# Optimization experiments

Hardware: AMD Instinct MI355X
Metric: run time of the kernel (lower is better)

Reference implementation:

```python
import jax, jax.numpy as jnp
import numpy as np

V = 50257; E = 1024; H = 1024; L = 256; NL = 2; D = 10


def setup_inputs() -> dict:
    key = jax.random.key(0)
    ks = jax.random.split(key, 16)
    n = lambda k, s: jax.random.normal(k, s, dtype=jnp.float32)
    return {
        "input_tok": jax.random.randint(ks[0], (1, 1), 0, V),
        "h0": n(ks[1], (NL, 1, H)),
        "c0": n(ks[2], (NL, 1, H)),
        "h_s": n(ks[3], (L, 1, H)),
        "h_t_tilde": n(ks[4], (1, 1, H)),
        "emb": n(ks[5], (V, E)) * 0.02,
        "Wp": n(ks[6], (H, H)) * (H ** -0.5),
        "wdot": n(ks[7], (1, H)) * (H ** -0.5),
        "Wbil": n(ks[8], (1, H, H)) * (H ** -0.5),
        "Wcomb": n(ks[9], (H, 2 * H)) * ((2 * H) ** -0.5),
        "bcomb": jnp.zeros((H,), jnp.float32),
        "Wih0": n(ks[10], (4 * H, E + H)) * ((E + H) ** -0.5),
        "Whh0": n(ks[11], (4 * H, H)) * (H ** -0.5),
        "bih0": jnp.zeros((4 * H,), jnp.float32),
        "bhh0": jnp.zeros((4 * H,), jnp.float32),
        "Wih1": n(ks[12], (4 * H, H)) * (H ** -0.5),
        "Whh1": n(ks[13], (4 * H, H)) * (H ** -0.5),
        "bih1": jnp.zeros((4 * H,), jnp.float32),
        "bhh1": jnp.zeros((4 * H,), jnp.float32),
        "Wout": n(ks[14], (V, H)) * (H ** -0.5),
        "bout": jnp.zeros((V,), jnp.float32),
    }


def _lstm_cell(x, h, c, Wih, Whh, bih, bhh):
    # torch LSTM gate order: i, f, g, o
    g = x @ Wih.T + bih + h @ Whh.T + bhh
    i, f, gg, o = jnp.split(g, 4, axis=-1)
    c2 = jax.nn.sigmoid(f) * c + jax.nn.sigmoid(i) * jnp.tanh(gg)
    h2 = jax.nn.sigmoid(o) * jnp.tanh(c2)
    return h2, c2


def reference(input_tok, h0, c0, h_s, h_t_tilde, emb, Wp, wdot, Wbil, Wcomb, bcomb,
              Wih0, Whh0, bih0, bhh0, Wih1, Whh1, bih1, bhh1, Wout, bout):
    embedding = emb[input_tok]                                  # [1,1,E]
    x = jnp.concatenate((embedding, h_t_tilde), axis=-1)[0]     # [1,E+H]
    h1, c1 = _lstm_cell(x, h0[0], c0[0], Wih0, Whh0, bih0, bhh0)
    h2, c2 = _lstm_cell(h1, h0[1], c0[1], Wih1, Whh1, bih1, bhh1)
    h_new = jnp.stack((h1, h2)); c_new = jnp.stack((c1, c2))
    h_t = h2                                                    # [1,H]
    Ls = h_s.shape[0]
    p_t = Ls * jax.nn.sigmoid(jnp.tanh(h_t @ Wp.T) @ wdot.T).squeeze()  # scalar
    s = jnp.round(p_t).astype(jnp.int32)
    idx = jnp.arange(Ls)
    lo = jnp.maximum(s - D, 0); hi = jnp.minimum(s + D, Ls - 1)
    mask = (idx >= lo) & (idx <= hi)                            # [L] local window
    # bilinear score h_t^T W h_s over all positions; mask outside window
    score = jnp.einsum('bh,ohk,lbk->lbo', h_t, Wbil, h_s)       # [L,1,1]
    neg = jnp.finfo(score.dtype).min
    a = jax.nn.softmax(jnp.where(mask[:, None, None], score, neg), axis=0)
    # NOTE: original uses exp(+d^2/(D/2)^2) (no minus sign); replicated faithfully.
    expo = jnp.where(mask, ((idx.astype(jnp.float32) - p_t) ** 2) / ((D / 2) ** 2), 0.0)
    a_t = a * jnp.exp(expo)[:, None, None]                      # [L,1,1]
    win = (hi - lo + 1).astype(jnp.float32)
    context = jnp.sum(a_t * h_s, axis=0, keepdims=True) / win   # [1,1,H] (mean over window)
    cat = jnp.concatenate((context, h_t[None]), axis=-1)        # [1,1,2H]
    h_t_tilde_new = jnp.tanh(cat @ Wcomb.T + bcomb)             # [1,1,H]
    y = jax.nn.log_softmax(h_t_tilde_new @ Wout.T + bout, axis=-1)  # [1,1,V]
    return (y, h_new, c_new, h_t_tilde_new, a_t, p_t)
```

## Files before the change

### kernel.cpp

```cpp
#include <hip/hip_runtime.h>
#include <math.h>

#define V 50257
#define E 1024
#define HH 1024
#define LL 256

#define O_H  (V)
#define O_C  (V + 2*HH)
#define O_HT (V + 4*HH)
#define O_A  (V + 5*HH)
#define O_P  (V + 5*HH + LL)

#define W_T    0
#define W_V    1024
#define W_H1   2048
#define W_H2   3072
#define W_Z    4096
#define W_BM   54400
#define W_BS   55424

#define NWL   8192
#define MAXR  7

__device__ __forceinline__ float sigmoidf_(float x) { return 1.f / (1.f + expf(-x)); }
__device__ __forceinline__ float dot4(float4 a, float4 b) {
    return a.x * b.x + a.y * b.y + a.z * b.z + a.w * b.w;
}

__device__ __forceinline__ float block_sum(float v, float* red) {
    int lane = threadIdx.x & 63, wv = threadIdx.x >> 6;
#pragma unroll
    for (int o = 32; o > 0; o >>= 1) v += __shfl_down(v, o, 64);
    __syncthreads();
    if (lane == 0) red[wv] = v;
    __syncthreads();
    return red[0] + red[1] + red[2] + red[3];
}

__global__ __launch_bounds__(512) void k_lstmA(
    const float* __restrict__ Wih0, const float* __restrict__ Whh0,
    const float* __restrict__ Whh1,
    const float* __restrict__ bih0, const float* __restrict__ bhh0,
    const float* __restrict__ emb, const int* __restrict__ tok,
    const float* __restrict__ htt,
    const float* __restrict__ h0, const float* __restrict__ c0,
    float* __restrict__ h1o, float* __restrict__ c1o, float* __restrict__ h1w,
    float* __restrict__ p1, float* __restrict__ vzero) {
    const int u = blockIdx.x, tid = threadIdx.x;
    if (tid == 0) vzero[u] = 0.f;
    const float4* xa4 = (const float4*)(emb + (size_t)tok[0] * E);
    const float4* xb4 = (const float4*)htt;
    const float4* r0 = (const float4*)(Wih0 + (size_t)u * 2048);
    const float4* r1 = (const float4*)(Wih0 + (size_t)(u + HH) * 2048);
    const float4* r2 = (const float4*)(Wih0 + (size_t)(u + 2*HH) * 2048);
    const float4* r3 = (const float4*)(Wih0 + (size_t)(u + 3*HH) * 2048);
    float4 xv = (tid < 256) ? xa4[tid] : xb4[tid - 256];
    float a0 = dot4(r0[tid], xv), a1 = dot4(r1[tid], xv);
    float a2 = dot4(r2[tid], xv), a3 = dot4(r3[tid], xv);
    float b0 = 0.f, b1 = 0.f, b2 = 0.f, b3 = 0.f;
    if (tid < 256) {
        const float4* s0 = (const float4*)(Whh0 + (size_t)u * HH);
        const float4* s1 = (const float4*)(Whh0 + (size_t)(u + HH) * HH);
        const float4* s2 = (const float4*)(Whh0 + (size_t)(u + 2*HH) * HH);
        const float4* s3 = (const float4*)(Whh0 + (size_t)(u + 3*HH) * HH);
        float4 hv = ((const float4*)h0)[tid];
        a0 += dot4(s0[tid], hv); a1 += dot4(s1[tid], hv);
        a2 += dot4(s2[tid], hv); a3 += dot4(s3[tid], hv);
    } else {
        int j = tid - 256;
        const float4* t0 = (const float4*)(Whh1 + (size_t)u * HH);
        const float4* t1 = (const float4*)(Whh1 + (size_t)(u + HH) * HH);
        const float4* t2 = (const float4*)(Whh1 + (size_t)(u + 2*HH) * HH);
        const float4* t3 = (const float4*)(Whh1 + (size_t)(u + 3*HH) * HH);
        float4 gv = ((const float4*)(h0 + HH))[j];
        b0 = dot4(t0[j], gv); b1 = dot4(t1[j], gv);
        b2 = dot4(t2[j], gv); b3 = dot4(t3[j], gv);
    }
    const int lane = tid & 63, wv = tid >> 6;
#pragma unroll
    for (int o = 32; o > 0; o >>= 1) {
        a0 += __shfl_down(a0, o, 64); a1 += __shfl_down(a1, o, 64);
        a2 += __shfl_down(a2, o, 64); a3 += __shfl_down(a3, o, 64);
        b0 += __shfl_down(b0, o, 64); b1 += __shfl_down(b1, o, 64);
        b2 += __shfl_down(b2, o, 64); b3 += __shfl_down(b3, o, 64);
    }
    __shared__ float sma[8][4], smb[8][4];
    if (lane == 0) {
        sma[wv][0] = a0; sma[wv][1] = a1; sma[wv][2] = a2; sma[wv][3] = a3;
        smb[wv][0] = b0; smb[wv][1] = b1; smb[wv][2] = b2; smb[wv][3] = b3;
    }
    __syncthreads();
    if (tid == 0) {
        float g[4], p[4];
#pragma unroll
        for (int i = 0; i < 4; ++i) {
            float ga = 0.f, pb = 0.f;
#pragma unroll
            for (int w = 0; w < 8; ++w) { ga += sma[w][i]; pb += smb[w][i]; }
            g[i] = ga + bih0[u + i*HH] + bhh0[u + i*HH];
            p[i] = pb;
        }
        float c = sigmoidf_(g[1]) * c0[u] + sigmoidf_(g[0]) * tanhf(g[2]);
        float h = sigmoidf_(g[3]) * tanhf(c);
        h1o[u] = h; c1o[u] = c; h1w[u] = h;
        p1[u*4+0] = p[0]; p1[u*4+1] = p[1]; p1[u*4+2] = p[2]; p1[u*4+3] = p[3];
    }
}

__global__ void k_lstmB(
    const float* __restrict__ Wih1,
    const float* __restrict__ bih1, const float* __restrict__ bhh1,
    const float* __restrict__ h1w, const float* __restrict__ p1,
    const float* __restrict__ h0, const float* __restrict__ c0,
    float* __restrict__ h2o, float* __restrict__ c2o, float* __restrict__ h2w) {
    const int u = blockIdx.x, tid = threadIdx.x;
    const float4* r0 = (const float4*)(Wih1 + (size_t)u * HH);
    const float4* r1 = (const float4*)(Wih1 + (size_t)(u + HH) * HH);
    const float4* r2 = (const float4*)(Wih1 + (size_t)(u + 2*HH) * HH);
    const float4* r3 = (const float4*)(Wih1 + (size_t)(u + 3*HH) * HH);
    float4 hv = ((const float4*)h1w)[tid];
    float a0 = dot4(r0[tid], hv), a1 = dot4(r1[tid], hv);
    float a2 = dot4(r2[tid], hv), a3 = dot4(r3[tid], hv);
    const int lane = tid & 63, wv = tid >> 6;
#pragma unroll
    for (int o = 32; o > 0; o >>= 1) {
        a0 += __shfl_down(a0, o, 64); a1 += __shfl_down(a1, o, 64);
        a2 += __shfl_down(a2, o, 64); a3 += __shfl_down(a3, o, 64);
    }
    __shared__ float sm[4][4];
    if (lane == 0) { sm[wv][0] = a0; sm[wv][1] = a1; sm[wv][2] = a2; sm[wv][3] = a3; }
    __syncthreads();
    if (tid == 0) {
        float g[4];
#pragma unroll
        for (int i = 0; i < 4; ++i)
            g[i] = sm[0][i] + sm[1][i] + sm[2][i] + sm[3][i]
                 + p1[u*4+i] + bih1[u + i*HH] + bhh1[u + i*HH];
        float c = sigmoidf_(g[1]) * c0[HH + u] + sigmoidf_(g[0]) * tanhf(g[2]);
        float h = sigmoidf_(g[3]) * tanhf(c);
        h2o[u] = h; c2o[u] = c; h2w[u] = h;
    }
}

__global__ void k_ptv(const float* __restrict__ Wp, const float* __restrict__ Wbil,
                      const float* __restrict__ h2, float* __restrict__ t_out,
                      float* __restrict__ v_out) {
    __shared__ float red[4];
    if (blockIdx.x < HH) {
        int r = blockIdx.x;
        const float4* row = (const float4*)(Wp + (size_t)r * HH);
        const float4* h24 = (const float4*)h2;
        float acc = dot4(row[threadIdx.x], h24[threadIdx.x]);
        float tot = block_sum(acc, red);
        if (threadIdx.x == 0) t_out[r] = tanhf(tot);
    } else {
        int b = blockIdx.x - HH;
        int h0 = b * 32;
        int k4 = threadIdx.x;
        const float4* W4 = (const float4*)Wbil;
        float4 acc = make_float4(0.f, 0.f, 0.f, 0.f);
        for (int h = h0; h < h0 + 32; ++h) {
            float hv = h2[h];
            float4 w = W4[(size_t)h * 256 + k4];
            acc.x += hv * w.x; acc.y += hv * w.y;
            acc.z += hv * w.z; acc.w += hv * w.w;
        }
        atomicAdd(&v_out[k4 * 4 + 0], acc.x);
        atomicAdd(&v_out[k4 * 4 + 1], acc.y);
        atomicAdd(&v_out[k4 * 4 + 2], acc.z);
        atomicAdd(&v_out[k4 * 4 + 3], acc.w);
    }
}

__global__ void k_combattn(const float* __restrict__ wdot, const float* __restrict__ t,
                           const float* __restrict__ v, const float* __restrict__ hs,
                           const float* __restrict__ h2, const float* __restrict__ Wcomb,
                           const float* __restrict__ bcomb,
                           float* __restrict__ outv, float* __restrict__ outv2,
                           float* __restrict__ ato, float* __restrict__ pto) {
    const int u = blockIdx.x, tid = threadIdx.x;
    const int lane = tid & 63, wv = tid >> 6;
    __shared__ float red[4];
    __shared__ float ssc[32];
    __shared__ float sa[LL];
    float p;
    {
        const float4* w4 = (const float4*)wdot;
        const float4* t4 = (const float4*)t;
        float acc = dot4(w4[tid], t4[tid]);
        p = (float)LL * sigmoidf_(block_sum(acc, red));
    }
    if (u == 0 && tid == 0) pto[0] = p;
    const int si = (int)rintf(p);
    const int lo = max(si - 10, 0), hi = min(si + 10, LL - 1);
    const int W = hi - lo + 1;
    const float4* v4 = (const float4*)v;
    for (int l = lo + wv; l <= hi; l += 4) {
        const float4* row = (const float4*)(hs + (size_t)l * HH);
        float a = 0.f;
#pragma unroll
        for (int j = lane; j < 256; j += 64) a += dot4(row[j], v4[j]);
#pragma unroll
        for (int o = 32; o > 0; o >>= 1) a += __shfl_xor(a, o, 64);
        if (lane == 0) ssc[l - lo] = a;
    }
    __syncthreads();
    float M = -INFINITY;
    for (int i = 0; i < W; ++i) M = fmaxf(M, ssc[i]);
    float S = 0.f;
    for (int i = 0; i < W; ++i) S += expf(ssc[i] - M);
    {
        bool mask = (tid >= lo) && (tid <= hi);
        int wi = min(max(tid - lo, 0), 31);
        float e = mask ? expf(ssc[wi] - M) : 0.f;
        float d = (float)tid - p;
        float at = mask ? (e / S) * expf(d * d * 0.04f) : 0.f;
        sa[tid] = at;
        if (u == 0) ato[tid] = at;
    }
    __syncthreads();
    const float4* hs4 = (const float4*)hs;
    float4 c = make_float4(0.f, 0.f, 0.f, 0.f);
    for (int l = lo; l <= hi; ++l) {
        float a = sa[l];
        float4 hv = hs4[(size_t)l * 256 + tid];
        c.x += a * hv.x; c.y += a * hv.y; c.z += a * hv.z; c.w += a * hv.w;
    }
    const float inv_win = 1.f / (float)W;
    c.x *= inv_win; c.y *= inv_win; c.z *= inv_win; c.w *= inv_win;
    {
        const float4* row = (const float4*)(Wcomb + (size_t)u * (2 * HH));
        const float4* h24 = (const float4*)h2;
        float acc = dot4(row[tid], c) + dot4(row[256 + tid], h24[tid]);
        float tot = block_sum(acc, red);
        if (tid == 0) {
            float h = tanhf(tot + bcomb[u]);
            outv[u] = h; outv2[u] = h;
        }
    }
}

__global__ __launch_bounds__(512) void k_logits(
    const float* __restrict__ Wout, const float* __restrict__ bout,
    const float* __restrict__ x, float* __restrict__ z,
    float* __restrict__ bmax, float* __restrict__ bsum) {
    const int tid = threadIdx.x, lane = tid & 63, wvi = tid >> 6;
    const int w = blockIdx.x * 8 + wvi;
    const float4* x4 = (const float4*)x;
    float4 x0 = x4[lane], x1 = x4[lane + 64], x2 = x4[lane + 128], x3 = x4[lane + 192];
    float m = -INFINITY, s = 0.f;
    for (int i = 0; i < MAXR; ++i) {
        int r = w + i * NWL;
        if (r < V) {
            const float4* row = (const float4*)(Wout + (size_t)r * 1024) + lane;
            float acc = dot4(row[0], x0) + dot4(row[64], x1)
                      + dot4(row[128], x2) + dot4(row[192], x3);
#pragma unroll
            for (int o = 32; o > 0; o >>= 1) acc += __shfl_xor(acc, o, 64);
            float zz = acc + bout[r];
            if (lane == 0) z[r] = zz;
            if (zz > m) { s *= expf(m - zz); m = zz; }
            s += expf(zz - m);
        }
    }
    __shared__ float wm[8], wsv[8];
    if (lane == 0) { wm[wvi] = m; wsv[wvi] = s; }
    __syncthreads();
    if (tid == 0) {
        float M = -INFINITY;
#pragma unroll
        for (int q = 0; q < 8; ++q) M = fmaxf(M, wm[q]);
        float S = 0.f;
        if (M != -INFINITY) {
#pragma unroll
            for (int q = 0; q < 8; ++q)
                if (wm[q] != -INFINITY) S += wsv[q] * expf(wm[q] - M);
        }
        bmax[blockIdx.x] = M; bsum[blockIdx.x] = S;
    }
}

__global__ void k_sub(const float* __restrict__ z, const float* __restrict__ bmax,
                      const float* __restrict__ bsum, float* __restrict__ y) {
    int tid = threadIdx.x;
    float m = -INFINITY, s = 0.f;
    for (int i = tid; i < 1024; i += 256) {
        float m2 = bmax[i], s2 = bsum[i];
        float M = fmaxf(m, m2);
        if (M != -INFINITY) s = s * expf(m - M) + s2 * expf(m2 - M);
        m = M;
    }
    int lane = tid & 63, wv = tid >> 6;
#pragma unroll
    for (int o = 32; o > 0; o >>= 1) {
        float m2 = __shfl_down(m, o, 64), s2 = __shfl_down(s, o, 64);
        float M = fmaxf(m, m2);
        if (M != -INFINITY) s = s * expf(m - M) + s2 * expf(m2 - M);
        else s = 0.f;
        m = M;
    }
    __shared__ float wm[4], wsv[4];
    __shared__ float lzs;
    if (lane == 0) { wm[wv] = m; wsv[wv] = s; }
    __syncthreads();
    if (tid == 0) {
        float M = -INFINITY, S = 0.f;
#pragma unroll
        for (int q = 0; q < 4; ++q) {
            float M2 = fmaxf(M, wm[q]);
            if (M2 != -INFINITY) S = S * expf(M - M2) + wsv[q] * expf(wm[q] - M2);
            M = M2;
        }
        lzs = M + logf(S);
    }
    __syncthreads();
    float lz = lzs;
    int i = blockIdx.x * 256 + tid;
    if (i < V) y[i] = z[i] - lz;
}

extern "C" void kernel_launch(void* const* d_in, const int* in_sizes, int n_in,
                              void* d_out, int out_size, void* d_ws, size_t ws_size,
                              hipStream_t stream) {
    const int*   tok   = (const int*)  d_in[0];
    const float* h0    = (const float*)d_in[1];
    const float* c0    = (const float*)d_in[2];
    const float* hs    = (const float*)d_in[3];
    const float* htt   = (const float*)d_in[4];
    const float* emb   = (const float*)d_in[5];
    const float* Wp    = (const float*)d_in[6];
    const float* wdot  = (const float*)d_in[7];
    const float* Wbil  = (const float*)d_in[8];
    const float* Wcomb = (const float*)d_in[9];
    const float* bcomb = (const float*)d_in[10];
    const float* Wih0  = (const float*)d_in[11];
    const float* Whh0  = (const float*)d_in[12];
    const float* bih0  = (const float*)d_in[13];
    const float* bhh0  = (const float*)d_in[14];
    const float* Wih1  = (const float*)d_in[15];
    const float* Whh1  = (const float*)d_in[16];
    const float* bih1  = (const float*)d_in[17];
    const float* bhh1  = (const float*)d_in[18];
    const float* Wout  = (const float*)d_in[19];
    const float* bout  = (const float*)d_in[20];

    float* out = (float*)d_out;
    float* ws  = (float*)d_ws;

    float* h1o  = out + O_H;
    float* h2o  = out + O_H + HH;
    float* c1o  = out + O_C;
    float* c2o  = out + O_C + HH;
    float* htto = out + O_HT;
    float* ato  = out + O_A;
    float* pto  = out + O_P;
    float* p1   = out;

    hipLaunchKernelGGL(k_lstmA, dim3(1024), dim3(512), 0, stream,
                       Wih0, Whh0, Whh1, bih0, bhh0, emb, tok, htt, h0, c0,
                       h1o, c1o, ws + W_H1, p1, ws + W_V);
    hipLaunchKernelGGL(k_lstmB, dim3(1024), dim3(256), 0, stream,
                       Wih1, bih1, bhh1, ws + W_H1, p1, h0, c0,
                       h2o, c2o, ws + W_H2);
    hipLaunchKernelGGL(k_ptv, dim3(1024 + 32), dim3(256), 0, stream,
                       Wp, Wbil, ws + W_H2, ws + W_T, ws + W_V);
    hipLaunchKernelGGL(k_combattn, dim3(1024), dim3(256), 0, stream,
                       wdot, ws + W_T, ws + W_V, hs, ws + W_H2, Wcomb, bcomb,
                       htto, ws + W_H1, ato, pto);
    hipLaunchKernelGGL(k_logits, dim3(1024), dim3(512), 0, stream,
                       Wout, bout, ws + W_H1, ws + W_Z, ws + W_BM, ws + W_BS);
    hipLaunchKernelGGL(k_sub, dim3((V + 255) / 256), dim3(256), 0, stream,
                       ws + W_Z, ws + W_BM, ws + W_BS, out);
}
```

Baseline: 84.92 us.

## Restructure logits kernel with contiguous row ranges, row prefetch, and max-free softmax sum

```diff
diff --git a/kernel.cpp b/kernel.cpp
--- a/kernel.cpp
+++ b/kernel.cpp
@@ -17,11 +17,9 @@
 #define W_H1   2048
 #define W_H2   3072
 #define W_Z    4096
-#define W_BM   54400
-#define W_BS   55424
-
-#define NWL   8192
-#define MAXR  7
+#define W_BS   54400
+
+#define NBL   2048
 
 __device__ __forceinline__ float sigmoidf_(float x) { return 1.f / (1.f + expf(-x)); }
 __device__ __forceinline__ float dot4(float4 a, float4 b) {
@@ -241,81 +239,58 @@
     }
 }
 
-__global__ __launch_bounds__(512) void k_logits(
-    const float* __restrict__ Wout, const float* __restrict__ bout,
-    const float* __restrict__ x, float* __restrict__ z,
-    float* __restrict__ bmax, float* __restrict__ bsum) {
-    const int tid = threadIdx.x, lane = tid & 63, wvi = tid >> 6;
-    const int w = blockIdx.x * 8 + wvi;
+__global__ void k_logits(const float* __restrict__ Wout, const float* __restrict__ bout,
+                         const float* __restrict__ x, float* __restrict__ z,
+                         float* __restrict__ bsum) {
+    const int b = blockIdx.x, tid = threadIdx.x;
+    const int lane = tid & 63, wvi = tid >> 6;
+    const int start = b * 24 + min(b, 1105);
+    const int cnt = 24 + (b < 1105 ? 1 : 0);
+    const int rend = start + cnt;
     const float4* x4 = (const float4*)x;
     float4 x0 = x4[lane], x1 = x4[lane + 64], x2 = x4[lane + 128], x3 = x4[lane + 192];
-    float m = -INFINITY, s = 0.f;
-    for (int i = 0; i < MAXR; ++i) {
-        int r = w + i * NWL;
-        if (r < V) {
-            const float4* row = (const float4*)(Wout + (size_t)r * 1024) + lane;
-            float acc = dot4(row[0], x0) + dot4(row[64], x1)
-                      + dot4(row[128], x2) + dot4(row[192], x3);
-#pragma unroll
-            for (int o = 32; o > 0; o >>= 1) acc += __shfl_xor(acc, o, 64);
-            float zz = acc + bout[r];
-            if (lane == 0) z[r] = zz;
-            if (zz > m) { s *= expf(m - zz); m = zz; }
-            s += expf(zz - m);
+    float s = 0.f;
+    int r = start + wvi;
+    float4 c0, c1, c2, c3;
+    bool has = r < rend;
+    if (has) {
+        const float4* rp = (const float4*)(Wout + (size_t)r * 1024) + lane;
+        c0 = rp[0]; c1 = rp[64]; c2 = rp[128]; c3 = rp[192];
+    }
+    while (has) {
+        const int rn = r + 4;
+        const bool hasn = rn < rend;
+        float4 n0, n1, n2, n3;
+        if (hasn) {
+            const float4* np = (const float4*)(Wout + (size_t)rn * 1024) + lane;
+            n0 = np[0]; n1 = np[64]; n2 = np[128]; n3 = np[192];
         }
-    }
-    __shared__ float wm[8], wsv[8];
-    if (lane == 0) { wm[wvi] = m; wsv[wvi] = s; }
-    __syncthreads();
-    if (tid == 0) {
-        float M = -INFINITY;
-#pragma unroll
-        for (int q = 0; q < 8; ++q) M = fmaxf(M, wm[q]);
-        float S = 0.f;
-        if (M != -INFINITY) {
-#pragma unroll
-            for (int q = 0; q < 8; ++q)
-                if (wm[q] != -INFINITY) S += wsv[q] * expf(wm[q] - M);
-        }
-        bmax[blockIdx.x] = M; bsum[blockIdx.x] = S;
-    }
-}
-
-__global__ void k_sub(const float* __restrict__ z, const float* __restrict__ bmax,
-                      const float* __restrict__ bsum, float* __restrict__ y) {
-    int tid = threadIdx.x;
-    float m = -INFINITY, s = 0.f;
-    for (int i = tid; i < 1024; i += 256) {
-        float m2 = bmax[i], s2 = bsum[i];
-        float M = fmaxf(m, m2);
-        if (M != -INFINITY) s = s * expf(m - M) + s2 * expf(m2 - M);
-        m = M;
-    }
-    int lane = tid & 63, wv = tid >> 6;
-#pragma unroll
-    for (int o = 32; o > 0; o >>= 1) {
-        float m2 = __shfl_down(m, o, 64), s2 = __shfl_down(s, o, 64);
-        float M = fmaxf(m, m2);
-        if (M != -INFINITY) s = s * expf(m - M) + s2 * expf(m2 - M);
-        else s = 0.f;
-        m = M;
-    }
-    __shared__ float wm[4], wsv[4];
+        float acc = dot4(c0, x0) + dot4(c1, x1) + dot4(c2, x2) + dot4(c3, x3);
+#pragma unroll
+        for (int o = 32; o > 0; o >>= 1) acc += __shfl_xor(acc, o, 64);
+        float zz = acc + bout[r];
+        if (lane == 0) z[r] = zz;
+        s += expf(zz);
+        r = rn; has = hasn;
+        c0 = n0; c1 = n1; c2 = n2; c3 = n3;
+    }
+    __shared__ float wsv[4];
+    if (lane == 0) wsv[wvi] = s;
+    __syncthreads();
+    if (tid == 0) bsum[b] = wsv[0] + wsv[1] + wsv[2] + wsv[3];
+}
+
+__global__ void k_sub(const float* __restrict__ z, const float* __restrict__ bsum,
+                      float* __restrict__ y) {
+    const int tid = threadIdx.x;
+    __shared__ float red[4];
     __shared__ float lzs;
-    if (lane == 0) { wm[wv] = m; wsv[wv] = s; }
-    __syncthreads();
-    if (tid == 0) {
-        float M = -INFINITY, S = 0.f;
-#pragma unroll
-        for (int q = 0; q < 4; ++q) {
-            float M2 = fmaxf(M, wm[q]);
-            if (M2 != -INFINITY) S = S * expf(M - M2) + wsv[q] * expf(wm[q] - M2);
-            M = M2;
-        }
-        lzs = M + logf(S);
-    }
-    __syncthreads();
-    float lz = lzs;
+    float s = 0.f;
+    for (int i = tid; i < NBL; i += 256) s += bsum[i];
+    float S = block_sum(s, red);
+    if (tid == 0) lzs = logf(S);
+    __syncthreads();
+    const float lz = lzs;
     int i = blockIdx.x * 256 + tid;
     if (i < V) y[i] = z[i] - lz;
 }
@@ -368,8 +343,8 @@
     hipLaunchKernelGGL(k_combattn, dim3(1024), dim3(256), 0, stream,
                        wdot, ws + W_T, ws + W_V, hs, ws + W_H2, Wcomb, bcomb,
                        htto, ws + W_H1, ato, pto);
-    hipLaunchKernelGGL(k_logits, dim3(1024), dim3(512), 0, stream,
-                       Wout, bout, ws + W_H1, ws + W_Z, ws + W_BM, ws + W_BS);
+    hipLaunchKernelGGL(k_logits, dim3(NBL), dim3(256), 0, stream,
+                       Wout, bout, ws + W_H1, ws + W_Z, ws + W_BS);
     hipLaunchKernelGGL(k_sub, dim3((V + 255) / 256), dim3(256), 0, stream,
-                       ws + W_Z, ws + W_BM, ws + W_BS, out);
-}
+                       ws + W_Z, ws + W_BS, out);
+}
```

New measurement: 85.47 us. No clear change (+0.6%).
